# Kernel tuning notes

Hardware: AMD Instinct MI355X
Metric: run time of the kernel (lower is better)

The kernel has to match this reference:

```python
import jax, jax.numpy as jnp
import numpy as np

N_NODES = 50000
N_EDGES = 800000
F_IN = 32
H = 128
N_REL = 4
MAX_DEG = 10
N_GRAPHS = 64
N_BLOCKS = 2


def setup_inputs() -> dict:
    key = jax.random.key(0)
    ks = jax.random.split(key, 20)
    s = 0.05
    return {
        "x": jax.random.normal(ks[0], (N_NODES, F_IN), jnp.float32),
        "edge_index": jax.random.randint(ks[1], (2, N_EDGES), 0, N_NODES, dtype=jnp.int32),
        "edge_attr": jax.random.randint(ks[2], (N_EDGES,), 0, N_REL, dtype=jnp.int32),
        "batch_idx": jnp.sort(jax.random.randint(ks[3], (N_NODES,), 0, N_GRAPHS, dtype=jnp.int32)),
        "embed_W": jax.random.normal(ks[4], (F_IN, H), jnp.float32) * s,
        "embed_b": jax.random.normal(ks[5], (H,), jnp.float32) * s,
        "rgcn_Wrel": jax.random.normal(ks[6], (N_BLOCKS, N_REL, H, H), jnp.float32) * s,
        "rgcn_Wroot": jax.random.normal(ks[7], (N_BLOCKS, H, H), jnp.float32) * s,
        "rgcn_b": jax.random.normal(ks[8], (N_BLOCKS, H), jnp.float32) * s,
        "mf_Wl": jax.random.normal(ks[9], (N_BLOCKS, MAX_DEG + 1, H, H), jnp.float32) * s,
        "mf_bl": jax.random.normal(ks[10], (N_BLOCKS, MAX_DEG + 1, H), jnp.float32) * s,
        "mf_Wr": jax.random.normal(ks[11], (N_BLOCKS, MAX_DEG + 1, H, H), jnp.float32) * s,
        "lin1_W": jax.random.normal(ks[12], (H, H), jnp.float32) * s,
        "lin1_b": jax.random.normal(ks[13], (H,), jnp.float32) * s,
        "lin2_W": jax.random.normal(ks[14], (H, 1), jnp.float32) * s,
        "lin2_b": jax.random.normal(ks[15], (1,), jnp.float32) * s,
    }


def _rgcn(x, src, dst, rel, Wrel, Wroot, b):
    # PyG RGCNConv with default aggr='mean': per-relation mean over incoming
    # edges, then per-relation weight, plus root transform and bias.
    seg = dst * N_REL + rel  # composite segment id: (node, relation)
    agg = jax.ops.segment_sum(x[src], seg, num_segments=N_NODES * N_REL)
    cnt = jax.ops.segment_sum(jnp.ones((seg.shape[0],), x.dtype), seg,
                              num_segments=N_NODES * N_REL)
    agg = (agg / jnp.maximum(cnt, 1.0)[:, None]).reshape(N_NODES, N_REL, H)
    return jnp.einsum('nrh,rho->no', agg, Wrel) + x @ Wroot + b


def _mfconv(x, src, dst, Wl, bl, Wr):
    # PyG MFConv: sum-aggregate neighbors, then per-degree-bucket linear heads
    # (degree = in-degree clamped to MAX_DEG); lin_r applied to root x (no bias).
    h = jax.ops.segment_sum(x[src], dst, num_segments=N_NODES)  # [N,H]
    deg = jax.ops.segment_sum(jnp.ones((src.shape[0],), jnp.int32), dst,
                              num_segments=N_NODES)
    deg = jnp.minimum(deg, MAX_DEG)  # [N]
    # out_all: [D+1, N, H] candidate outputs, one per degree bucket
    out_all = (jnp.einsum('nh,dho->dno', h, Wl)
               + jnp.einsum('nh,dho->dno', x, Wr)
               + bl[:, None, :])
    return jnp.take_along_axis(out_all, deg[None, :, None], axis=0)[0]


def reference(x, edge_index, edge_attr, batch_idx, embed_W, embed_b,
              rgcn_Wrel, rgcn_Wroot, rgcn_b, mf_Wl, mf_bl, mf_Wr,
              lin1_W, lin1_b, lin2_W, lin2_b):
    src, dst = edge_index[0], edge_index[1]
    h = x @ embed_W + embed_b
    for blk in range(N_BLOCKS):
        if blk > 0:  # first block uses Identity instead of ReLU
            h = jax.nn.relu(h)
        h = _rgcn(h, src, dst, edge_attr, rgcn_Wrel[blk], rgcn_Wroot[blk], rgcn_b[blk])
        h = jax.nn.relu(h)
        h = _mfconv(h, src, dst, mf_Wl[blk], mf_bl[blk], mf_Wr[blk])
    g = jax.ops.segment_sum(h, batch_idx, num_segments=N_GRAPHS)  # global_add_pool
    g = jax.nn.relu(g @ lin1_W + lin1_b)
    return g @ lin2_W + lin2_b
```

## Files before the change

### kernel.cpp

```cpp
#include <hip/hip_runtime.h>
#include <hip/hip_bf16.h>

#define NRELS 4
#define MAXDEG 10
#define NBUCK 11
#define POOL_CHUNKS 8

typedef __attribute__((ext_vector_type(8))) short s16x8;
typedef __attribute__((ext_vector_type(4))) float f32x4;
typedef __attribute__((ext_vector_type(8))) unsigned short u16x8;

__device__ inline unsigned short f2b(float f) {
  __hip_bfloat16 h = __float2bfloat16(f);
  return *reinterpret_cast<unsigned short*>(&h);
}
__device__ inline float b2f(unsigned short u) {
  union { unsigned int i; float f; } v;
  v.i = ((unsigned int)u) << 16;
  return v.f;
}
__device__ inline float blo(unsigned int v) {
  union { unsigned int i; float f; } x;
  x.i = v << 16;
  return x.f;
}
__device__ inline float bhi(unsigned int v) {
  union { unsigned int i; float f; } x;
  x.i = v & 0xffff0000u;
  return x.f;
}

typedef __attribute__((address_space(3))) unsigned int lds_uint;
typedef __attribute__((address_space(1))) const unsigned int glob_uint;
__device__ __forceinline__ void gld_lds16(const void* g, void* l) {
  __builtin_amdgcn_global_load_lds((glob_uint*)g, (lds_uint*)l, 16, 0, 0);
}

__global__ __launch_bounds__(512) void coarse_count(const int* __restrict__ dst,
                                                    int* __restrict__ bhist, int E) {
  __shared__ int lh[512];
  int t = threadIdx.x;
  lh[t] = 0;
  __syncthreads();
  int base = blockIdx.x * 4096;
  int lim = E - base;
  if (lim > 4096) lim = 4096;
  for (int i = t; i < lim; i += 512) atomicAdd(&lh[dst[base + i] >> 7], 1);
  __syncthreads();
  if (lh[t]) atomicAdd(&bhist[t], lh[t]);
}

__global__ __launch_bounds__(512) void coarse_scan(const int* __restrict__ bhist,
                                                   int* __restrict__ boff,
                                                   int* __restrict__ bcur, int NB, int E) {
  __shared__ int sd[512];
  int t = threadIdx.x;
  int v = (t < NB) ? bhist[t] : 0;
  sd[t] = v;
  __syncthreads();
  for (int o = 1; o < 512; o <<= 1) {
    int x = (t >= o) ? sd[t - o] : 0;
    __syncthreads();
    sd[t] += x;
    __syncthreads();
  }
  if (t < NB) {
    int st = sd[t] - v;
    boff[t] = st;
    bcur[t] = st;
  }
  if (t == 0) boff[NB] = E;
}

__global__ __launch_bounds__(512) void coarse_scatter(
    const int* __restrict__ src, const int* __restrict__ dst, const int* __restrict__ rel,
    int* __restrict__ bcur, uint2* __restrict__ ebuf, int E) {
  __shared__ int lhist[512];
  __shared__ int lstart[512];
  __shared__ int lcur[512];
  __shared__ int gbase[512];
  __shared__ uint2 stage[4096];
  int t = threadIdx.x;
  lhist[t] = 0;
  __syncthreads();
  int base = blockIdx.x * 4096;
  int lim = E - base;
  if (lim > 4096) lim = 4096;
  for (int i = t; i < lim; i += 512) atomicAdd(&lhist[dst[base + i] >> 7], 1);
  __syncthreads();
  int myc = lhist[t];
  lstart[t] = myc;
  __syncthreads();
  for (int o = 1; o < 512; o <<= 1) {
    int x = (t >= o) ? lstart[t - o] : 0;
    __syncthreads();
    lstart[t] += x;
    __syncthreads();
  }
  int incl = lstart[t];
  __syncthreads();
  lstart[t] = incl - myc;
  lcur[t] = 0;
  if (myc > 0) gbase[t] = atomicAdd(&bcur[t], myc);
  __syncthreads();
  for (int i = t; i < lim; i += 512) {
    int e = base + i;
    int d = dst[e];
    int b = d >> 7;
    int slot = lstart[b] + atomicAdd(&lcur[b], 1);
    stage[slot] = make_uint2((unsigned)(d * 4 + rel[e]), (unsigned)src[e]);
  }
  __syncthreads();
  for (int i = t; i < lim; i += 512) {
    uint2 val = stage[i];
    int b = (int)(val.x >> 9);
    ebuf[gbase[b] + (i - lstart[b])] = val;
  }
}

__global__ __launch_bounds__(512) void fine_count_scan(
    const uint2* __restrict__ ebuf, const int* __restrict__ boff, int* __restrict__ cnt,
    int* __restrict__ seg_start, float* __restrict__ inv, int* __restrict__ deg,
    int* __restrict__ bucket, int* __restrict__ hist, int NSEG) {
  __shared__ int lh[512];
  __shared__ int sc[512];
  __shared__ int lbh[16];
  int t = threadIdx.x;
  int b = blockIdx.x;
  lh[t] = 0;
  if (t < 16) lbh[t] = 0;
  __syncthreads();
  int s = boff[b], e = boff[b + 1];
  for (int i = s + t; i < e; i += 512) atomicAdd(&lh[ebuf[i].x & 511], 1);
  __syncthreads();
  int v = lh[t];
  sc[t] = v;
  __syncthreads();
  for (int o = 1; o < 512; o <<= 1) {
    int x = (t >= o) ? sc[t - o] : 0;
    __syncthreads();
    sc[t] += x;
    __syncthreads();
  }
  int gseg = b * 512 + t;
  if (gseg < NSEG) {
    cnt[gseg] = v;
    seg_start[gseg] = s + sc[t] - v;
    inv[gseg] = 1.0f / (float)(v > 1 ? v : 1);
    if ((t & 3) == 0) {
      int d = sc[t + 3] - sc[t] + v;
      int n = gseg >> 2;
      deg[n] = d;
      int bk = d < MAXDEG ? d : MAXDEG;
      bucket[n] = bk;
      atomicAdd(&lbh[bk], 1);
    }
  }
  __syncthreads();
  if (t < NBUCK && lbh[t]) atomicAdd(&hist[t], lbh[t]);
}

__global__ __launch_bounds__(512) void place_local(const uint2* __restrict__ ebuf,
                                                   const int* __restrict__ boff,
                                                   const int* __restrict__ seg_start,
                                                   int* __restrict__ csr, int NSEG) {
  __shared__ int lcur[512];
  int t = threadIdx.x;
  int b = blockIdx.x;
  int gseg = b * 512 + t;
  lcur[t] = (gseg < NSEG) ? seg_start[gseg] : 0;
  __syncthreads();
  int s = boff[b], e = boff[b + 1];
  for (int i = s + t; i < e; i += 512) {
    uint2 v = ebuf[i];
    int pos = atomicAdd(&lcur[v.x & 511], 1);
    csr[pos] = (int)v.y;
  }
}

__global__ void calc_offsets(const int* __restrict__ hist, int* __restrict__ off,
                             int* __restrict__ fill) {
  if (threadIdx.x == 0) {
    int acc = 0;
    for (int b = 0; b < NBUCK; b++) {
      off[b] = acc;
      fill[b] = acc;
      acc += ((hist[b] + 63) >> 6) << 6;
    }
    off[NBUCK] = acc;
  }
}

__global__ void build_perm(const int* __restrict__ bucket, int* __restrict__ fill,
                           int* __restrict__ perm, int N) {
  int n = blockIdx.x * 256 + threadIdx.x;
  int b = (n < N) ? bucket[n] : -1;
  int lane = threadIdx.x & 63;
  for (int bb = 0; bb < NBUCK; bb++) {
    unsigned long long m = __ballot(b == bb);
    if (m == 0ULL) continue;
    int leader = __ffsll(m) - 1;
    int base = 0;
    if (lane == leader) base = atomicAdd(&fill[bb], __popcll(m));
    base = __shfl(base, leader);
    if (b == bb) {
      int idx = __popcll(m & ((1ULL << lane) - 1ULL));
      perm[base + idx] = n;
    }
  }
}

__global__ void conv_weights(const float* __restrict__ Wrel, const float* __restrict__ Wroot,
                             const float* __restrict__ Wl, const float* __restrict__ Wr,
                             const float* __restrict__ embW, unsigned short* __restrict__ Bt,
                             unsigned short* __restrict__ Btm, unsigned short* __restrict__ Bte) {
  const int R1 = 2 * 128 * 640;
  const int R2 = R1 + 2 * 11 * 128 * 256;
  const int R3 = R2 + 128 * 32;
  int t = blockIdx.x * 256 + threadIdx.x;
  if (t < R1) {
    int blk = t / 81920;
    int rem = t % 81920;
    int n = rem / 640;
    int k = rem % 640;
    float v;
    if (k < 512)
      v = Wrel[(size_t)blk * 65536 + (size_t)k * 128 + n];
    else
      v = Wroot[(size_t)blk * 16384 + (size_t)(k - 512) * 128 + n];
    Bt[t] = f2b(v);
    return;
  }
  if (t < R2) {
    int t2 = t - R1;
    int k = t2 & 255;
    int n = (t2 >> 8) & 127;
    int bb = (t2 >> 15) % 11;
    int blk = t2 / (11 * 128 * 256);
    float v;
    if (k < 128)
      v = Wl[(((size_t)blk * 11 + bb) * 128 + k) * 128 + n];
    else
      v = Wr[(((size_t)blk * 11 + bb) * 128 + (k - 128)) * 128 + n];
    Btm[t2] = f2b(v);
    return;
  }
  if (t < R3) {
    int t3 = t - R2;
    int n = t3 >> 5, k = t3 & 31;
    Bte[t3] = f2b(embW[(size_t)k * 128 + n]);
  }
}

#define ACC8(v)                                   \
  do {                                            \
    a0 += blo((v).x); a1 += bhi((v).x);           \
    a2 += blo((v).y); a3 += bhi((v).y);           \
    a4 += blo((v).z); a5 += bhi((v).z);           \
    a6 += blo((v).w); a7 += bhi((v).w);           \
  } while (0)

__global__ __launch_bounds__(256) void rgcn_gather(
    const unsigned short* __restrict__ hb, const int* __restrict__ csr,
    const int* __restrict__ seg_start, const int* __restrict__ cnt,
    const float* __restrict__ inv, const int* __restrict__ perm,
    unsigned short* __restrict__ ahat, int total) {
  int i = blockIdx.x * 16 + (threadIdx.x >> 4);
  if (i >= total) return;
  int n = perm[i];
  if (n < 0) return;
  int c8 = (threadIdx.x & 15) * 8;
#pragma unroll
  for (int r = 0; r < 4; r++) {
    int seg = n * 4 + r;
    int st = seg_start[seg], cn = cnt[seg];
    float w = inv[seg];
    float a0 = 0.f, a1 = 0.f, a2 = 0.f, a3 = 0.f, a4 = 0.f, a5 = 0.f, a6 = 0.f, a7 = 0.f;
    int ii = 0;
    for (; ii + 4 <= cn; ii += 4) {
      int p0 = csr[st + ii], p1 = csr[st + ii + 1];
      int p2 = csr[st + ii + 2], p3 = csr[st + ii + 3];
      uint4 v0 = *(const uint4*)(hb + (size_t)p0 * 128 + c8);
      uint4 v1 = *(const uint4*)(hb + (size_t)p1 * 128 + c8);
      uint4 v2 = *(const uint4*)(hb + (size_t)p2 * 128 + c8);
      uint4 v3 = *(const uint4*)(hb + (size_t)p3 * 128 + c8);
      ACC8(v0);
      ACC8(v1);
      ACC8(v2);
      ACC8(v3);
    }
    if (ii + 2 <= cn) {
      int p0 = csr[st + ii], p1 = csr[st + ii + 1];
      uint4 v0 = *(const uint4*)(hb + (size_t)p0 * 128 + c8);
      uint4 v1 = *(const uint4*)(hb + (size_t)p1 * 128 + c8);
      ACC8(v0);
      ACC8(v1);
      ii += 2;
    }
    if (ii < cn) {
      uint4 v0 = *(const uint4*)(hb + (size_t)csr[st + ii] * 128 + c8);
      ACC8(v0);
    }
    uint4 o;
    o.x = (unsigned int)f2b(a0 * w) | ((unsigned int)f2b(a1 * w) << 16);
    o.y = (unsigned int)f2b(a2 * w) | ((unsigned int)f2b(a3 * w) << 16);
    o.z = (unsigned int)f2b(a4 * w) | ((unsigned int)f2b(a5 * w) << 16);
    o.w = (unsigned int)f2b(a6 * w) | ((unsigned int)f2b(a7 * w) << 16);
    *(uint4*)(ahat + (size_t)i * 512 + r * 128 + c8) = o;
  }
}

__global__ __launch_bounds__(256) void mf_gather(
    const unsigned short* __restrict__ hb, const int* __restrict__ csr,
    const int* __restrict__ seg_start, const int* __restrict__ deg,
    const int* __restrict__ perm, unsigned short* __restrict__ amf, int total) {
  int i = blockIdx.x * 16 + (threadIdx.x >> 4);
  if (i >= total) return;
  int c8 = (threadIdx.x & 15) * 8;
  int n = perm[i];
  if (n < 0) return;
  int st = seg_start[n * 4], dg = deg[n];
  float a0 = 0.f, a1 = 0.f, a2 = 0.f, a3 = 0.f, a4 = 0.f, a5 = 0.f, a6 = 0.f, a7 = 0.f;
  int i2 = 0;
  for (; i2 + 4 <= dg; i2 += 4) {
    int p0 = csr[st + i2], p1 = csr[st + i2 + 1];
    int p2 = csr[st + i2 + 2], p3 = csr[st + i2 + 3];
    uint4 v0 = *(const uint4*)(hb + (size_t)p0 * 128 + c8);
    uint4 v1 = *(const uint4*)(hb + (size_t)p1 * 128 + c8);
    uint4 v2 = *(const uint4*)(hb + (size_t)p2 * 128 + c8);
    uint4 v3 = *(const uint4*)(hb + (size_t)p3 * 128 + c8);
    ACC8(v0);
    ACC8(v1);
    ACC8(v2);
    ACC8(v3);
  }
  if (i2 + 2 <= dg) {
    int p0 = csr[st + i2], p1 = csr[st + i2 + 1];
    uint4 v0 = *(const uint4*)(hb + (size_t)p0 * 128 + c8);
    uint4 v1 = *(const uint4*)(hb + (size_t)p1 * 128 + c8);
    ACC8(v0);
    ACC8(v1);
    i2 += 2;
  }
  if (i2 < dg) {
    uint4 v0 = *(const uint4*)(hb + (size_t)csr[st + i2] * 128 + c8);
    ACC8(v0);
  }
  uint4 o;
  o.x = (unsigned int)f2b(a0) | ((unsigned int)f2b(a1) << 16);
  o.y = (unsigned int)f2b(a2) | ((unsigned int)f2b(a3) << 16);
  o.z = (unsigned int)f2b(a4) | ((unsigned int)f2b(a5) << 16);
  o.w = (unsigned int)f2b(a6) | ((unsigned int)f2b(a7) << 16);
  *(uint4*)(amf + (size_t)i * 128 + c8) = o;
}

__global__ __launch_bounds__(256) void rgcn_mfma(const unsigned short* __restrict__ A,
                                                 const unsigned short* __restrict__ hroot,
                                                 const unsigned short* __restrict__ Bt,
                                                 const float* __restrict__ bias,
                                                 const int* __restrict__ perm,
                                                 unsigned short* __restrict__ out) {
  __shared__ unsigned char As[8192];
  __shared__ unsigned char Bs[16384];
  __shared__ int nodes[64];
  int t = threadIdx.x;
  int m0 = blockIdx.x * 64;
  if (t >= 64 && t < 128) nodes[t - 64] = perm[m0 + t - 64];
  __syncthreads();
  int lane = t & 63, wave = t >> 6;
  int row = lane & 15, quad = lane >> 4;
  int nh = wave * 32;
  f32x4 acc[2][4];
#pragma unroll
  for (int i = 0; i < 2; i++)
#pragma unroll
    for (int j = 0; j < 4; j++) acc[i][j] = (f32x4){0.f, 0.f, 0.f, 0.f};

  for (int kt = 0; kt < 10; kt++) {
    int kb2 = kt * 128;
#pragma unroll
    for (int s = 0; s < 2; s++) {
      int o = s * 4096 + t * 16;
      int r = o >> 7, c = ((o >> 4) & 7) ^ (r & 7);
      const char* gsrc;
      if (kt < 8) {
        gsrc = (const char*)A + (size_t)(m0 + r) * 1024 + kb2 + c * 16;
      } else {
        int nd = nodes[r];
        if (nd < 0) nd = 0;
        gsrc = (const char*)hroot + (size_t)nd * 256 + (kb2 - 1024) + c * 16;
      }
      gld_lds16(gsrc, As + o);
    }
#pragma unroll
    for (int s = 0; s < 4; s++) {
      int o = s * 4096 + t * 16;
      int r = o >> 7, c = ((o >> 4) & 7) ^ (r & 7);
      gld_lds16((const char*)Bt + (size_t)r * 1280 + kb2 + c * 16, Bs + o);
    }
    __syncthreads();
#pragma unroll
    for (int ks = 0; ks < 2; ks++) {
      int cch = ks * 4 + quad;
      s16x8 af[4], bf[2];
#pragma unroll
      for (int mt = 0; mt < 4; mt++) {
        int R = mt * 16 + row;
        af[mt] = *(const s16x8*)(As + R * 128 + ((cch ^ (R & 7)) << 4));
      }
#pragma unroll
      for (int nt = 0; nt < 2; nt++) {
        int R = nh + nt * 16 + row;
        bf[nt] = *(const s16x8*)(Bs + R * 128 + ((cch ^ (R & 7)) << 4));
      }
#pragma unroll
      for (int nt = 0; nt < 2; nt++)
#pragma unroll
        for (int mt = 0; mt < 4; mt++)
          acc[nt][mt] = __builtin_amdgcn_mfma_f32_16x16x32_bf16(af[mt], bf[nt], acc[nt][mt], 0, 0, 0);
    }
    __syncthreads();
  }
#pragma unroll
  for (int nt = 0; nt < 2; nt++) {
    int n = nh + nt * 16 + row;
    float bv = bias[n];
#pragma unroll
    for (int mt = 0; mt < 4; mt++) {
#pragma unroll
      for (int r4 = 0; r4 < 4; r4++) {
        int nd = nodes[mt * 16 + quad * 4 + r4];
        if (nd >= 0) out[(size_t)nd * 128 + n] = f2b(fmaxf(acc[nt][mt][r4] + bv, 0.f));
      }
    }
  }
}

__global__ __launch_bounds__(256) void mf_mfma(const unsigned short* __restrict__ A,
                                               const unsigned short* __restrict__ hroot,
                                               const unsigned short* __restrict__ Bt,
                                               const float* __restrict__ bl,
                                               const int* __restrict__ perm,
                                               const int* __restrict__ off,
                                               unsigned short* __restrict__ out, int relu_out) {
  __shared__ unsigned char As[8192];
  __shared__ unsigned char Bs[16384];
  __shared__ int soff[12];
  __shared__ int nodes[64];
  int t = threadIdx.x;
  int m0 = blockIdx.x * 64;
  if (t < 12) soff[t] = off[t];
  if (t >= 64 && t < 128) nodes[t - 64] = perm[m0 + t - 64];
  __syncthreads();
  if (m0 >= soff[11]) return;
  int b = 0;
  while (b < 10 && m0 >= soff[b + 1]) b++;
  const unsigned short* Bb = Bt + (size_t)b * 128 * 256;
  const float* bb = bl + b * 128;
  int lane = t & 63, wave = t >> 6;
  int row = lane & 15, quad = lane >> 4;
  int nh = wave * 32;
  f32x4 acc[2][4];
#pragma unroll
  for (int i = 0; i < 2; i++)
#pragma unroll
    for (int j = 0; j < 4; j++) acc[i][j] = (f32x4){0.f, 0.f, 0.f, 0.f};

  for (int kt = 0; kt < 4; kt++) {
    int kb2 = kt * 128;
#pragma unroll
    for (int s = 0; s < 2; s++) {
      int o = s * 4096 + t * 16;
      int r = o >> 7, c = ((o >> 4) & 7) ^ (r & 7);
      const char* gsrc;
      if (kt < 2) {
        gsrc = (const char*)A + (size_t)(m0 + r) * 256 + kb2 + c * 16;
      } else {
        int nd = nodes[r];
        if (nd < 0) nd = 0;
        gsrc = (const char*)hroot + (size_t)nd * 256 + (kb2 - 512) + c * 16;
      }
      gld_lds16(gsrc, As + o);
    }
#pragma unroll
    for (int s = 0; s < 4; s++) {
      int o = s * 4096 + t * 16;
      int r = o >> 7, c = ((o >> 4) & 7) ^ (r & 7);
      gld_lds16((const char*)Bb + (size_t)r * 512 + kb2 + c * 16, Bs + o);
    }
    __syncthreads();
#pragma unroll
    for (int ks = 0; ks < 2; ks++) {
      int cch = ks * 4 + quad;
      s16x8 af[4], bf[2];
#pragma unroll
      for (int mt = 0; mt < 4; mt++) {
        int R = mt * 16 + row;
        af[mt] = *(const s16x8*)(As + R * 128 + ((cch ^ (R & 7)) << 4));
      }
#pragma unroll
      for (int nt = 0; nt < 2; nt++) {
        int R = nh + nt * 16 + row;
        bf[nt] = *(const s16x8*)(Bs + R * 128 + ((cch ^ (R & 7)) << 4));
      }
#pragma unroll
      for (int nt = 0; nt < 2; nt++)
#pragma unroll
        for (int mt = 0; mt < 4; mt++)
          acc[nt][mt] = __builtin_amdgcn_mfma_f32_16x16x32_bf16(af[mt], bf[nt], acc[nt][mt], 0, 0, 0);
    }
    __syncthreads();
  }
#pragma unroll
  for (int nt = 0; nt < 2; nt++) {
    int n = nh + nt * 16 + row;
    float bv = bb[n];
#pragma unroll
    for (int mt = 0; mt < 4; mt++) {
#pragma unroll
      for (int r4 = 0; r4 < 4; r4++) {
        int nd = nodes[mt * 16 + quad * 4 + r4];
        if (nd >= 0) {
          float v = acc[nt][mt][r4] + bv;
          if (relu_out) v = fmaxf(v, 0.f);
          out[(size_t)nd * 128 + n] = f2b(v);
        }
      }
    }
  }
}

__global__ __launch_bounds__(256) void embed_mfma(const float* __restrict__ x,
                                                  const unsigned short* __restrict__ Bte,
                                                  const float* __restrict__ bias,
                                                  unsigned short* __restrict__ out, int N) {
  __shared__ unsigned char As[64 * 80];
  __shared__ unsigned char Bs[128 * 80];
  int t = threadIdx.x;
  int m0 = blockIdx.x * 64;
  {
    int r = t >> 2, s = t & 3;
    int gr = m0 + r;
    if (gr >= N) gr = N - 1;
    const float* xp = x + (size_t)gr * 32 + s * 8;
    float4 f0 = *(const float4*)xp;
    float4 f1 = *(const float4*)(xp + 4);
    u16x8 o;
    o[0] = f2b(f0.x); o[1] = f2b(f0.y); o[2] = f2b(f0.z); o[3] = f2b(f0.w);
    o[4] = f2b(f1.x); o[5] = f2b(f1.y); o[6] = f2b(f1.z); o[7] = f2b(f1.w);
    *(u16x8*)(As + r * 80 + s * 16) = o;
  }
  {
    int n = t >> 1, s = t & 1;
    const unsigned short* bp = Bte + (size_t)n * 32 + s * 16;
    uint4 v0 = *(const uint4*)bp;
    uint4 v1 = *(const uint4*)(bp + 8);
    *(uint4*)(Bs + n * 80 + s * 32) = v0;
    *(uint4*)(Bs + n * 80 + s * 32 + 16) = v1;
  }
  __syncthreads();
  int lane = t & 63, wave = t >> 6;
  int row = lane & 15, quad = lane >> 4;
  int nh = wave * 32;
  f32x4 acc[2][4];
#pragma unroll
  for (int i = 0; i < 2; i++)
#pragma unroll
    for (int j = 0; j < 4; j++) acc[i][j] = (f32x4){0.f, 0.f, 0.f, 0.f};
  s16x8 af[4], bf[2];
#pragma unroll
  for (int mt = 0; mt < 4; mt++) {
    int R = mt * 16 + row;
    af[mt] = *(const s16x8*)(As + R * 80 + quad * 16);
  }
#pragma unroll
  for (int nt = 0; nt < 2; nt++) {
    int R = nh + nt * 16 + row;
    bf[nt] = *(const s16x8*)(Bs + R * 80 + quad * 16);
  }
#pragma unroll
  for (int nt = 0; nt < 2; nt++)
#pragma unroll
    for (int mt = 0; mt < 4; mt++)
      acc[nt][mt] = __builtin_amdgcn_mfma_f32_16x16x32_bf16(af[mt], bf[nt], acc[nt][mt], 0, 0, 0);
#pragma unroll
  for (int nt = 0; nt < 2; nt++) {
    int n = nh + nt * 16 + row;
    float bv = bias[n];
#pragma unroll
    for (int mt = 0; mt < 4; mt++) {
#pragma unroll
      for (int r4 = 0; r4 < 4; r4++) {
        int m = m0 + mt * 16 + quad * 4 + r4;
        if (m < N) out[(size_t)m * 128 + n] = f2b(acc[nt][mt][r4] + bv);
      }
    }
  }
}

__global__ void pool2(const unsigned short* __restrict__ h, const int* __restrict__ batch,
                      float* __restrict__ g, int N, int G) {
  int gr = blockIdx.x / POOL_CHUNKS;
  int ck = blockIdx.x % POOL_CHUNKS;
  int c = threadIdx.x;
  int lo = 0, hi = N;
  while (lo < hi) {
    int m = (lo + hi) >> 1;
    if (batch[m] < gr) lo = m + 1; else hi = m;
  }
  int s = lo;
  lo = s; hi = N;
  while (lo < hi) {
    int m = (lo + hi) >> 1;
    if (batch[m] < gr + 1) lo = m + 1; else hi = m;
  }
  int e = lo;
  int len = e - s;
  int a = s + (int)(((long long)len * ck) / POOL_CHUNKS);
  int b = s + (int)(((long long)len * (ck + 1)) / POOL_CHUNKS);
  float sum = 0.f;
  for (int n = a; n < b; n++) sum += b2f(h[(size_t)n * 128 + c]);
  if (b > a) atomicAdd(&g[gr * 128 + c], sum);
}

__global__ void head_kernel(const float* __restrict__ g, const float* __restrict__ W1,
                            const float* __restrict__ b1, const float* __restrict__ W2,
                            const float* __restrict__ b2, float* __restrict__ out) {
  int bg = blockIdx.x;
  int o = threadIdx.x;
  __shared__ float gs[128];
  __shared__ float red[128];
  gs[o] = g[bg * 128 + o];
  __syncthreads();
  float acc = b1[o];
  for (int k = 0; k < 128; k++) acc += gs[k] * W1[k * 128 + o];
  acc = fmaxf(acc, 0.f);
  red[o] = acc * W2[o];
  __syncthreads();
  for (int s = 64; s > 0; s >>= 1) {
    if (o < s) red[o] += red[o + s];
    __syncthreads();
  }
  if (o == 0) out[bg] = red[0] + b2[0];
}

extern "C" void kernel_launch(void* const* d_in, const int* in_sizes, int n_in,
                              void* d_out, int out_size, void* d_ws, size_t ws_size,
                              hipStream_t stream) {
  const float* x = (const float*)d_in[0];
  const int* ei = (const int*)d_in[1];
  const int* ea = (const int*)d_in[2];
  const int* batch = (const int*)d_in[3];
  const float* embW = (const float*)d_in[4];
  const float* embB = (const float*)d_in[5];
  const float* Wrel = (const float*)d_in[6];
  const float* Wroot = (const float*)d_in[7];
  const float* rb = (const float*)d_in[8];
  const float* Wl = (const float*)d_in[9];
  const float* bl = (const float*)d_in[10];
  const float* Wr = (const float*)d_in[11];
  const float* l1W = (const float*)d_in[12];
  const float* l1b = (const float*)d_in[13];
  const float* l2W = (const float*)d_in[14];
  const float* l2b = (const float*)d_in[15];
  float* out = (float*)d_out;

  int N = in_sizes[0] / 32;
  int E = in_sizes[2];
  int G = out_size;
  int NSEG = N * 4;
  int NB = (N + 127) >> 7;

  char* p = (char*)d_ws;
  auto alloc = [&](size_t bytes) {
    char* r = p;
    p += (bytes + 255) & ~(size_t)255;
    return r;
  };
  int permCap = ((N + 63) / 64 + NBUCK) * 64;
  unsigned short* h_bf = (unsigned short*)alloc((size_t)N * 128 * 2);
  unsigned short* h2_bf = (unsigned short*)alloc((size_t)N * 128 * 2);
  unsigned short* ahat = (unsigned short*)alloc((size_t)permCap * 512 * 2);
  unsigned short* amf = (unsigned short*)alloc((size_t)permCap * 128 * 2);
  unsigned short* Btr = (unsigned short*)alloc((size_t)2 * 128 * 640 * 2);
  unsigned short* Btm = (unsigned short*)alloc((size_t)2 * 11 * 128 * 256 * 2);
  unsigned short* Bte = (unsigned short*)alloc((size_t)128 * 32 * 2);
  float* inv = (float*)alloc((size_t)NSEG * 4);
  int* cnt = (int*)alloc((size_t)NSEG * 4);
  int* seg_start = (int*)alloc((size_t)NSEG * 4);
  int* csr = (int*)alloc((size_t)E * 4);
  uint2* ebuf = (uint2*)alloc((size_t)E * 8);
  int* deg = (int*)alloc((size_t)N * 4);
  int* bucket = (int*)alloc((size_t)N * 4);
  int* perm = (int*)alloc((size_t)permCap * 4);
  int* boff = (int*)alloc(516 * 4);
  int* bcur = (int*)alloc(512 * 4);
  int* off = (int*)alloc(64);
  int* fill = (int*)alloc(64);
  size_t zeroBytes = 8192 + (size_t)G * 128 * 4;
  char* zb = alloc(zeroBytes);
  int* bhist = (int*)zb;
  int* hist = (int*)(zb + 4096);
  float* g = (float*)(zb + 8192);

  hipMemsetAsync(zb, 0, zeroBytes, stream);
  hipMemsetAsync(perm, 0xFF, (size_t)permCap * 4, stream);

  const int* src = ei;
  const int* dst = ei + E;

  int sblocks = (E + 4095) / 4096;
  coarse_count<<<sblocks, 512, 0, stream>>>(dst, bhist, E);
  coarse_scan<<<1, 512, 0, stream>>>(bhist, boff, bcur, NB, E);
  coarse_scatter<<<sblocks, 512, 0, stream>>>(src, dst, ea, bcur, ebuf, E);
  fine_count_scan<<<NB, 512, 0, stream>>>(ebuf, boff, cnt, seg_start, inv, deg, bucket, hist,
                                          NSEG);
  calc_offsets<<<1, 64, 0, stream>>>(hist, off, fill);
  build_perm<<<(N + 255) / 256, 256, 0, stream>>>(bucket, fill, perm, N);
  place_local<<<NB, 512, 0, stream>>>(ebuf, boff, seg_start, csr, NSEG);
  int convTotal = 2 * 128 * 640 + 2 * 11 * 128 * 256 + 128 * 32;
  conv_weights<<<(convTotal + 255) / 256, 256, 0, stream>>>(Wrel, Wroot, Wl, Wr, embW, Btr,
                                                            Btm, Bte);

  embed_mfma<<<(N + 63) / 64, 256, 0, stream>>>(x, Bte, embB, h_bf, N);

  int mfblocks = permCap / 64;
  for (int blk = 0; blk < 2; blk++) {
    rgcn_gather<<<(permCap + 15) / 16, 256, 0, stream>>>(h_bf, csr, seg_start, cnt, inv, perm,
                                                         ahat, permCap);
    rgcn_mfma<<<mfblocks, 256, 0, stream>>>(ahat, h_bf, Btr + (size_t)blk * 81920,
                                            rb + blk * 128, perm, h2_bf);
    mf_gather<<<(permCap + 15) / 16, 256, 0, stream>>>(h2_bf, csr, seg_start, deg, perm, amf,
                                                       permCap);
    mf_mfma<<<mfblocks, 256, 0, stream>>>(amf, h2_bf, Btm + (size_t)blk * 11 * 128 * 256,
                                          bl + (size_t)blk * 11 * 128, perm, off, h_bf,
                                          (blk == 0) ? 1 : 0);
  }
  pool2<<<G * POOL_CHUNKS, 128, 0, stream>>>(h_bf, batch, g, N, G);
  head_kernel<<<G, 128, 0, stream>>>(g, l1W, l1b, l2W, l2b, out);
}
```

Before: 408.6 us.

## Split gather work into feature halves and fold offset computation into consumers

After: 406.2 us. Within noise of the previous version (-0.6%).

```diff
diff --git a/kernel.cpp b/kernel.cpp
--- a/kernel.cpp
+++ b/kernel.cpp
@@ -178,21 +178,17 @@
   }
 }
 
-__global__ void calc_offsets(const int* __restrict__ hist, int* __restrict__ off,
-                             int* __restrict__ fill) {
+__global__ void build_perm(const int* __restrict__ bucket, const int* __restrict__ hist,
+                           int* __restrict__ fill, int* __restrict__ perm, int N) {
+  __shared__ int soff[NBUCK];
   if (threadIdx.x == 0) {
     int acc = 0;
     for (int b = 0; b < NBUCK; b++) {
-      off[b] = acc;
-      fill[b] = acc;
+      soff[b] = acc;
       acc += ((hist[b] + 63) >> 6) << 6;
     }
-    off[NBUCK] = acc;
-  }
-}
-
-__global__ void build_perm(const int* __restrict__ bucket, int* __restrict__ fill,
-                           int* __restrict__ perm, int N) {
+  }
+  __syncthreads();
   int n = blockIdx.x * 256 + threadIdx.x;
   int b = (n < N) ? bucket[n] : -1;
   int lane = threadIdx.x & 63;
@@ -205,7 +201,7 @@
     base = __shfl(base, leader);
     if (b == bb) {
       int idx = __popcll(m & ((1ULL << lane) - 1ULL));
-      perm[base + idx] = n;
+      perm[soff[bb] + base + idx] = n;
     }
   }
 }
@@ -265,11 +261,12 @@
     const int* __restrict__ seg_start, const int* __restrict__ cnt,
     const float* __restrict__ inv, const int* __restrict__ perm,
     unsigned short* __restrict__ ahat, int total) {
-  int i = blockIdx.x * 16 + (threadIdx.x >> 4);
+  int half = blockIdx.x & 1;
+  int i = (blockIdx.x >> 1) * 32 + (threadIdx.x >> 3);
   if (i >= total) return;
   int n = perm[i];
   if (n < 0) return;
-  int c8 = (threadIdx.x & 15) * 8;
+  int c8 = half * 64 + (threadIdx.x & 7) * 8;
 #pragma unroll
   for (int r = 0; r < 4; r++) {
     int seg = n * 4 + r;
@@ -314,11 +311,12 @@
     const unsigned short* __restrict__ hb, const int* __restrict__ csr,
     const int* __restrict__ seg_start, const int* __restrict__ deg,
     const int* __restrict__ perm, unsigned short* __restrict__ amf, int total) {
-  int i = blockIdx.x * 16 + (threadIdx.x >> 4);
+  int half = blockIdx.x & 1;
+  int i = (blockIdx.x >> 1) * 32 + (threadIdx.x >> 3);
   if (i >= total) return;
-  int c8 = (threadIdx.x & 15) * 8;
   int n = perm[i];
   if (n < 0) return;
+  int c8 = half * 64 + (threadIdx.x & 7) * 8;
   int st = seg_start[n * 4], dg = deg[n];
   float a0 = 0.f, a1 = 0.f, a2 = 0.f, a3 = 0.f, a4 = 0.f, a5 = 0.f, a6 = 0.f, a7 = 0.f;
   int i2 = 0;
@@ -441,18 +439,25 @@
                                                const unsigned short* __restrict__ Bt,
                                                const float* __restrict__ bl,
                                                const int* __restrict__ perm,
-                                               const int* __restrict__ off,
+                                               const int* __restrict__ hist,
                                                unsigned short* __restrict__ out, int relu_out) {
   __shared__ unsigned char As[8192];
   __shared__ unsigned char Bs[16384];
-  __shared__ int soff[12];
+  __shared__ int soff[NBUCK + 1];
   __shared__ int nodes[64];
   int t = threadIdx.x;
   int m0 = blockIdx.x * 64;
-  if (t < 12) soff[t] = off[t];
+  if (t == 0) {
+    int acc = 0;
+    for (int b2 = 0; b2 < NBUCK; b2++) {
+      soff[b2] = acc;
+      acc += ((hist[b2] + 63) >> 6) << 6;
+    }
+    soff[NBUCK] = acc;
+  }
   if (t >= 64 && t < 128) nodes[t - 64] = perm[m0 + t - 64];
   __syncthreads();
-  if (m0 >= soff[11]) return;
+  if (m0 >= soff[NBUCK]) return;
   int b = 0;
   while (b < 10 && m0 >= soff[b + 1]) b++;
   const unsigned short* Bb = Bt + (size_t)b * 128 * 256;
@@ -695,12 +700,11 @@
   int* perm = (int*)alloc((size_t)permCap * 4);
   int* boff = (int*)alloc(516 * 4);
   int* bcur = (int*)alloc(512 * 4);
-  int* off = (int*)alloc(64);
-  int* fill = (int*)alloc(64);
   size_t zeroBytes = 8192 + (size_t)G * 128 * 4;
   char* zb = alloc(zeroBytes);
   int* bhist = (int*)zb;
   int* hist = (int*)(zb + 4096);
+  int* fill = (int*)(zb + 4224);
   float* g = (float*)(zb + 8192);
 
   hipMemsetAsync(zb, 0, zeroBytes, stream);
@@ -715,8 +719,7 @@
   coarse_scatter<<<sblocks, 512, 0, stream>>>(src, dst, ea, bcur, ebuf, E);
   fine_count_scan<<<NB, 512, 0, stream>>>(ebuf, boff, cnt, seg_start, inv, deg, bucket, hist,
                                           NSEG);
-  calc_offsets<<<1, 64, 0, stream>>>(hist, off, fill);
-  build_perm<<<(N + 255) / 256, 256, 0, stream>>>(bucket, fill, perm, N);
+  build_perm<<<(N + 255) / 256, 256, 0, stream>>>(bucket, hist, fill, perm, N);
   place_local<<<NB, 512, 0, stream>>>(ebuf, boff, seg_start, csr, NSEG);
   int convTotal = 2 * 128 * 640 + 2 * 11 * 128 * 256 + 128 * 32;
   conv_weights<<<(convTotal + 255) / 256, 256, 0, stream>>>(Wrel, Wroot, Wl, Wr, embW, Btr,
@@ -725,15 +728,15 @@
   embed_mfma<<<(N + 63) / 64, 256, 0, stream>>>(x, Bte, embB, h_bf, N);
 
   int mfblocks = permCap / 64;
+  int gblocks = ((permCap + 31) / 32) * 2;
   for (int blk = 0; blk < 2; blk++) {
-    rgcn_gather<<<(permCap + 15) / 16, 256, 0, stream>>>(h_bf, csr, seg_start, cnt, inv, perm,
-                                                         ahat, permCap);
+    rgcn_gather<<<gblocks, 256, 0, stream>>>(h_bf, csr, seg_start, cnt, inv, perm, ahat,
+                                             permCap);
     rgcn_mfma<<<mfblocks, 256, 0, stream>>>(ahat, h_bf, Btr + (size_t)blk * 81920,
                                             rb + blk * 128, perm, h2_bf);
-    mf_gather<<<(permCap + 15) / 16, 256, 0, stream>>>(h2_bf, csr, seg_start, deg, perm, amf,
-                                                       permCap);
+    mf_gather<<<gblocks, 256, 0, stream>>>(h2_bf, csr, seg_start, deg, perm, amf, permCap);
     mf_mfma<<<mfblocks, 256, 0, stream>>>(amf, h2_bf, Btm + (size_t)blk * 11 * 128 * 256,
-                                          bl + (size_t)blk * 11 * 128, perm, off, h_bf,
+                                          bl + (size_t)blk * 11 * 128, perm, hist, h_bf,
                                           (blk == 0) ? 1 : 0);
   }
   pool2<<<G * POOL_CHUNKS, 128, 0, stream>>>(h_bf, batch, g, N, G);
```
